# Performance work log

Measured on AMD Instinct MI355X. Metric: run time of the kernel, lower is better.

Reference implementation:

```python
import jax, jax.numpy as jnp
import numpy as np

B, D_IN, RANK, UNITS = 8192, 4096, 2048, 4096

def setup_inputs() -> dict:
    key = jax.random.key(0)
    k1, k2, k3, k4 = jax.random.split(key, 4)
    inputs = jax.random.normal(k1, (B, D_IN), dtype=jnp.float32)
    U = jax.random.normal(k2, (D_IN, RANK), dtype=jnp.float32) / np.sqrt(D_IN)
    S = jax.random.uniform(k3, (RANK,), dtype=jnp.float32)
    V = jax.random.normal(k4, (UNITS, RANK), dtype=jnp.float32) / np.sqrt(UNITS)
    bias = jnp.zeros((UNITS,), dtype=jnp.float32)
    return {"inputs": inputs, "U": U, "S": S, "V": V, "bias": bias}

def reference(inputs, U, S, V, bias):
    # kernel = U @ diag(S) @ V^T; out = relu(inputs @ kernel + bias)
    # Computed in factored form (same math, avoids dense [D_IN, UNITS] kernel):
    h = (inputs @ U) * S            # [B, rank]
    out = h @ V.T + bias            # [B, units]
    return jax.nn.relu(out)
```

## Files before the change

### kernel.cpp

```cpp
#include <hip/hip_runtime.h>
#include <hip/hip_bf16.h>

#define BSZ   8192
#define DIN   4096
#define RNK   2048
#define UNT   4096

typedef __attribute__((ext_vector_type(4))) float  f32x4;
typedef __attribute__((ext_vector_type(8))) float  f32x8;
typedef __attribute__((ext_vector_type(8))) short  s16x8;
typedef __attribute__((ext_vector_type(8))) unsigned short u16x8;

typedef unsigned short u16;

__device__ __forceinline__ u16 f2bf(float f) {
    unsigned int u = __builtin_bit_cast(unsigned int, f);
    return (u16)((u + 0x7fffu + ((u >> 16) & 1u)) >> 16);
}

__global__ void cvt_bf16_kernel(const float* __restrict__ x,
                                u16* __restrict__ y, int n8) {
    int i = blockIdx.x * blockDim.x + threadIdx.x;
    if (i >= n8) return;
    f32x8 v = ((const f32x8*)x)[i];
    u16x8 o;
#pragma unroll
    for (int j = 0; j < 8; ++j) o[j] = f2bf(v[j]);
    ((u16x8*)y)[i] = o;
}

__global__ void transpose_scale_kernel(const float* __restrict__ U,
                                       const float* __restrict__ S,
                                       u16* __restrict__ Ut) {
    __shared__ float tile[32][33];
    const int r0 = blockIdx.x * 32;
    const int k0 = blockIdx.y * 32;
    const int tx = threadIdx.x;
    const int ty = threadIdx.y;
#pragma unroll
    for (int i = 0; i < 32; i += 8)
        tile[ty + i][tx] = U[(size_t)(k0 + ty + i) * RNK + r0 + tx];
    __syncthreads();
#pragma unroll
    for (int i = 0; i < 32; i += 8) {
        int r = r0 + ty + i;
        Ut[(size_t)r * DIN + k0 + tx] = f2bf(tile[tx][ty + i] * S[r]);
    }
}

__device__ __forceinline__ void glds16(const void* g, void* l) {
    __builtin_amdgcn_global_load_lds(
        (const __attribute__((address_space(1))) unsigned int*)g,
        (__attribute__((address_space(3))) unsigned int*)l,
        16, 0, 0);
}

template <int K, bool RELU_BIAS>
__global__ __launch_bounds__(256) void gemm_bt(
    const u16* __restrict__ A, const u16* __restrict__ Bt,
    void* __restrict__ C, const float* __restrict__ bias, int N) {
    __shared__ u16 As[2][128 * 32];
    __shared__ u16 Bs[2][128 * 32];

    const int t    = threadIdx.x;
    const int wave = t >> 6;
    const int lane = t & 63;

    const int rowBase = blockIdx.y * 128;
    const int colBase = blockIdx.x * 128;

    const int sRow = t >> 2;
    const int sCol = (t & 3) * 8;
    const u16* aG = A  + (size_t)(rowBase + sRow) * K + sCol;
    const u16* bG = Bt + (size_t)(colBase + sRow) * K + sCol;
    const int lo = sRow * 32 + sCol;
    const int hi = (sRow + 64) * 32 + sCol;

    const int wm = (wave >> 1) * 64;
    const int wn = (wave & 1) * 64;
    const int fr = lane & 15;
    const int fk = (lane >> 4) * 8;

    const int fOff = (wm + fr) * 32 + fk;
    const int gOff = (wn + fr) * 32 + fk;

    f32x4 acc[4][4] = {};

    for (int k0 = 0; k0 < K; k0 += 64) {
        __syncthreads();
        glds16(aG + k0,                       &As[0][lo]);
        glds16(aG + (size_t)64 * K + k0,      &As[0][hi]);
        glds16(aG + k0 + 32,                  &As[1][lo]);
        glds16(aG + (size_t)64 * K + k0 + 32, &As[1][hi]);
        glds16(bG + k0,                       &Bs[0][lo]);
        glds16(bG + (size_t)64 * K + k0,      &Bs[0][hi]);
        glds16(bG + k0 + 32,                  &Bs[1][lo]);
        glds16(bG + (size_t)64 * K + k0 + 32, &Bs[1][hi]);
        __syncthreads();

#pragma unroll
        for (int h = 0; h < 2; ++h) {
            const u16* aF = &As[h][fOff];
            const u16* bF = &Bs[h][gOff];
            s16x8 af[4], bf[4];
#pragma unroll
            for (int i = 0; i < 4; ++i) af[i] = *(const s16x8*)(aF + i * 16 * 32);
#pragma unroll
            for (int j = 0; j < 4; ++j) bf[j] = *(const s16x8*)(bF + j * 16 * 32);
#pragma unroll
            for (int i = 0; i < 4; ++i)
#pragma unroll
                for (int j = 0; j < 4; ++j)
                    acc[i][j] = __builtin_amdgcn_mfma_f32_16x16x32_bf16(
                        af[i], bf[j], acc[i][j], 0, 0, 0);
        }
    }

    const int cRow = rowBase + wm + (lane >> 4) * 4;
    const int cCol = colBase + wn + fr;
    if (RELU_BIAS) {
        float* Cf = (float*)C;
#pragma unroll
        for (int j = 0; j < 4; ++j) {
            const int col = cCol + j * 16;
            const float bv = bias[col];
#pragma unroll
            for (int i = 0; i < 4; ++i) {
#pragma unroll
                for (int r = 0; r < 4; ++r) {
                    float v = acc[i][j][r] + bv;
                    Cf[(size_t)(cRow + i * 16 + r) * N + col] = v > 0.f ? v : 0.f;
                }
            }
        }
    } else {
        u16* Cb = (u16*)C;
#pragma unroll
        for (int j = 0; j < 4; ++j) {
            const int col = cCol + j * 16;
#pragma unroll
            for (int i = 0; i < 4; ++i) {
#pragma unroll
                for (int r = 0; r < 4; ++r)
                    Cb[(size_t)(cRow + i * 16 + r) * N + col] = f2bf(acc[i][j][r]);
            }
        }
    }
}

extern "C" void kernel_launch(void* const* d_in, const int* in_sizes, int n_in,
                              void* d_out, int out_size, void* d_ws, size_t ws_size,
                              hipStream_t stream) {
    const float* X    = (const float*)d_in[0];
    const float* U    = (const float*)d_in[1];
    const float* S    = (const float*)d_in[2];
    const float* V    = (const float*)d_in[3];
    const float* bias = (const float*)d_in[4];
    float* out = (float*)d_out;

    char* ws = (char*)d_ws;
    u16* Xb  = (u16*)ws;
    u16* Utb = (u16*)(ws + ((size_t)64 << 20));
    u16* Vb  = (u16*)(ws + ((size_t)80 << 20));
    u16* Hb  = (u16*)(ws + ((size_t)96 << 20));

    {
        int n8 = (BSZ * DIN) / 8;
        cvt_bf16_kernel<<<n8 / 256, 256, 0, stream>>>(X, Xb, n8);
    }
    {
        dim3 grid(RNK / 32, DIN / 32), block(32, 8);
        transpose_scale_kernel<<<grid, block, 0, stream>>>(U, S, Utb);
    }
    {
        int n8 = (UNT * RNK) / 8;
        cvt_bf16_kernel<<<n8 / 256, 256, 0, stream>>>(V, Vb, n8);
    }
    {
        dim3 grid(RNK / 128, BSZ / 128);
        gemm_bt<DIN, false><<<grid, 256, 0, stream>>>(Xb, Utb, Hb, nullptr, RNK);
    }
    {
        dim3 grid(UNT / 128, BSZ / 128);
        gemm_bt<RNK, true><<<grid, 256, 0, stream>>>(Hb, Vb, out, bias, UNT);
    }
}
```

Baseline: 569.3 us.

## Replace 128x128 GEMM with 256x256 tile, 8-wave pipelined swizzled kernel

Rewrites the bf16 GEMM kernel to use 256x256 output tiles with 512 threads and a K step of 64. The LDS layout is XOR-swizzled to avoid bank conflicts, and global-to-LDS prefetch is staggered across four MFMA phases with barriers and raised wave priority. Workgroup IDs are remapped for better L2 locality. The aim is to raise arithmetic intensity and overlap loads with MFMA, at the cost of 128KB of LDS and higher register pressure, which may limit occupancy.

```diff
diff --git a/kernel.cpp b/kernel.cpp
--- a/kernel.cpp
+++ b/kernel.cpp
@@ -56,93 +56,183 @@
 }
 
 template <int K, bool RELU_BIAS>
-__global__ __launch_bounds__(256) void gemm_bt(
+__global__ __launch_bounds__(512) void gemm256(
     const u16* __restrict__ A, const u16* __restrict__ Bt,
     void* __restrict__ C, const float* __restrict__ bias, int N) {
-    __shared__ u16 As[2][128 * 32];
-    __shared__ u16 Bs[2][128 * 32];
-
-    const int t    = threadIdx.x;
+    __shared__ u16 As[2][256 * 64];
+    __shared__ u16 Bs[2][256 * 64];
+
+    const int t = threadIdx.x;
+
+    const int gx = gridDim.x;
+    const int nwg = gx * gridDim.y;
+    int bid = blockIdx.y * gx + blockIdx.x;
+    bid = (bid & 7) * (nwg >> 3) + (bid >> 3);
+    const int rowBase = (bid / gx) * 256;
+    const int colBase = (bid % gx) * 256;
+
+    const int sRow = t >> 3;
+    const int sCol = ((t & 7) ^ (sRow & 7)) << 3;
+    const u16* aS = A  + (size_t)(rowBase + sRow) * K + sCol;
+    const u16* bS = Bt + (size_t)(colBase + sRow) * K + sCol;
+
+#define STG(SRC, DST, h_, Tk_, b_) do {                                       \
+    const u16* s_ = (SRC) + (size_t)(h_) * 128 * K + (size_t)(Tk_) * 64;      \
+    glds16(s_,                  &DST[b_][(h_) * 8192 + t * 8]);               \
+    glds16(s_ + (size_t)64 * K, &DST[b_][(h_) * 8192 + 4096 + t * 8]);        \
+} while (0)
+
+    const int lane = t & 63;
     const int wave = t >> 6;
-    const int lane = t & 63;
-
-    const int rowBase = blockIdx.y * 128;
-    const int colBase = blockIdx.x * 128;
-
-    const int sRow = t >> 2;
-    const int sCol = (t & 3) * 8;
-    const u16* aG = A  + (size_t)(rowBase + sRow) * K + sCol;
-    const u16* bG = Bt + (size_t)(colBase + sRow) * K + sCol;
-    const int lo = sRow * 32 + sCol;
-    const int hi = (sRow + 64) * 32 + sCol;
-
-    const int wm = (wave >> 1) * 64;
-    const int wn = (wave & 1) * 64;
-    const int fr = lane & 15;
-    const int fk = (lane >> 4) * 8;
-
-    const int fOff = (wm + fr) * 32 + fk;
-    const int gOff = (wn + fr) * 32 + fk;
-
-    f32x4 acc[4][4] = {};
-
-    for (int k0 = 0; k0 < K; k0 += 64) {
-        __syncthreads();
-        glds16(aG + k0,                       &As[0][lo]);
-        glds16(aG + (size_t)64 * K + k0,      &As[0][hi]);
-        glds16(aG + k0 + 32,                  &As[1][lo]);
-        glds16(aG + (size_t)64 * K + k0 + 32, &As[1][hi]);
-        glds16(bG + k0,                       &Bs[0][lo]);
-        glds16(bG + (size_t)64 * K + k0,      &Bs[0][hi]);
-        glds16(bG + k0 + 32,                  &Bs[1][lo]);
-        glds16(bG + (size_t)64 * K + k0 + 32, &Bs[1][hi]);
-        __syncthreads();
-
-#pragma unroll
-        for (int h = 0; h < 2; ++h) {
-            const u16* aF = &As[h][fOff];
-            const u16* bF = &Bs[h][gOff];
-            s16x8 af[4], bf[4];
-#pragma unroll
-            for (int i = 0; i < 4; ++i) af[i] = *(const s16x8*)(aF + i * 16 * 32);
-#pragma unroll
-            for (int j = 0; j < 4; ++j) bf[j] = *(const s16x8*)(bF + j * 16 * 32);
-#pragma unroll
-            for (int i = 0; i < 4; ++i)
-#pragma unroll
-                for (int j = 0; j < 4; ++j)
-                    acc[i][j] = __builtin_amdgcn_mfma_f32_16x16x32_bf16(
-                        af[i], bf[j], acc[i][j], 0, 0, 0);
-        }
-    }
-
-    const int cRow = rowBase + wm + (lane >> 4) * 4;
-    const int cCol = colBase + wn + fr;
+    const int wm = wave >> 2;
+    const int wn = wave & 3;
+    const int lr = lane & 15;
+    const int lg = lane >> 4;
+    const int r7 = lr & 7;
+    const int swz0 = ((lg    ) ^ r7) << 4;
+    const int swz1 = ((lg + 4) ^ r7) << 4;
+    const int aRowB = (wm * 128 + lr) * 128;
+    const int bRowB = (wn * 64  + lr) * 128;
+
+    f32x4 acc[8][4] = {};
+    s16x8 af[8][2], bf[2][2];
+
+    STG(aS, As, 0, 0, 0); STG(aS, As, 1, 0, 0);
+    STG(bS, Bs, 0, 0, 0); STG(bS, Bs, 1, 0, 0);
+    STG(aS, As, 0, 1, 1); STG(aS, As, 1, 1, 1);
+    asm volatile("s_waitcnt vmcnt(4)" ::: "memory");
+    __builtin_amdgcn_s_barrier();
+
+    const int NT = K / 64;
+    for (int T = 0; T < NT; ++T) {
+        const int cur = T & 1, nxt = cur ^ 1;
+        const char* aP = (const char*)&As[cur][0] + aRowB;
+        const char* bP = (const char*)&Bs[cur][0] + bRowB;
+
+#pragma unroll
+        for (int mi = 0; mi < 4; ++mi) {
+            af[mi][0] = *(const s16x8*)(aP + mi * 2048 + swz0);
+            af[mi][1] = *(const s16x8*)(aP + mi * 2048 + swz1);
+        }
+#pragma unroll
+        for (int nj = 0; nj < 2; ++nj) {
+            bf[nj][0] = *(const s16x8*)(bP + nj * 2048 + swz0);
+            bf[nj][1] = *(const s16x8*)(bP + nj * 2048 + swz1);
+        }
+        if (T + 1 < NT) STG(bS, Bs, 0, T + 1, nxt);
+        asm volatile("" ::: "memory");
+        __builtin_amdgcn_s_barrier();
+        asm volatile("s_waitcnt lgkmcnt(0)" ::: "memory");
+        __builtin_amdgcn_sched_barrier(0);
+        __builtin_amdgcn_s_setprio(1);
+#pragma unroll
+        for (int mi = 0; mi < 4; ++mi)
+#pragma unroll
+            for (int nj = 0; nj < 2; ++nj)
+#pragma unroll
+                for (int kk = 0; kk < 2; ++kk)
+                    acc[mi][nj] = __builtin_amdgcn_mfma_f32_16x16x32_bf16(
+                        af[mi][kk], bf[nj][kk], acc[mi][nj], 0, 0, 0);
+        __builtin_amdgcn_s_setprio(0);
+        asm volatile("" ::: "memory");
+        __builtin_amdgcn_s_barrier();
+
+#pragma unroll
+        for (int mi = 0; mi < 4; ++mi) {
+            af[4 + mi][0] = *(const s16x8*)(aP + (4 + mi) * 2048 + swz0);
+            af[4 + mi][1] = *(const s16x8*)(aP + (4 + mi) * 2048 + swz1);
+        }
+        if (T + 1 < NT) STG(bS, Bs, 1, T + 1, nxt);
+        asm volatile("" ::: "memory");
+        __builtin_amdgcn_s_barrier();
+        asm volatile("s_waitcnt lgkmcnt(0)" ::: "memory");
+        __builtin_amdgcn_sched_barrier(0);
+        __builtin_amdgcn_s_setprio(1);
+#pragma unroll
+        for (int mi = 0; mi < 4; ++mi)
+#pragma unroll
+            for (int nj = 0; nj < 2; ++nj)
+#pragma unroll
+                for (int kk = 0; kk < 2; ++kk)
+                    acc[4 + mi][nj] = __builtin_amdgcn_mfma_f32_16x16x32_bf16(
+                        af[4 + mi][kk], bf[nj][kk], acc[4 + mi][nj], 0, 0, 0);
+        __builtin_amdgcn_s_setprio(0);
+        asm volatile("" ::: "memory");
+        __builtin_amdgcn_s_barrier();
+
+#pragma unroll
+        for (int nj = 0; nj < 2; ++nj) {
+            bf[nj][0] = *(const s16x8*)(bP + (2 + nj) * 2048 + swz0);
+            bf[nj][1] = *(const s16x8*)(bP + (2 + nj) * 2048 + swz1);
+        }
+        if (T + 2 < NT) STG(aS, As, 0, T + 2, cur);
+        asm volatile("" ::: "memory");
+        __builtin_amdgcn_s_barrier();
+        asm volatile("s_waitcnt lgkmcnt(0)" ::: "memory");
+        __builtin_amdgcn_sched_barrier(0);
+        __builtin_amdgcn_s_setprio(1);
+#pragma unroll
+        for (int mi = 0; mi < 4; ++mi)
+#pragma unroll
+            for (int nj = 0; nj < 2; ++nj)
+#pragma unroll
+                for (int kk = 0; kk < 2; ++kk)
+                    acc[mi][2 + nj] = __builtin_amdgcn_mfma_f32_16x16x32_bf16(
+                        af[mi][kk], bf[nj][kk], acc[mi][2 + nj], 0, 0, 0);
+        __builtin_amdgcn_s_setprio(0);
+        asm volatile("" ::: "memory");
+        __builtin_amdgcn_s_barrier();
+
+        if (T + 2 < NT) STG(aS, As, 1, T + 2, cur);
+        asm volatile("" ::: "memory");
+        __builtin_amdgcn_s_barrier();
+        __builtin_amdgcn_s_setprio(1);
+#pragma unroll
+        for (int mi = 0; mi < 4; ++mi)
+#pragma unroll
+            for (int nj = 0; nj < 2; ++nj)
+#pragma unroll
+                for (int kk = 0; kk < 2; ++kk)
+                    acc[4 + mi][2 + nj] = __builtin_amdgcn_mfma_f32_16x16x32_bf16(
+                        af[4 + mi][kk], bf[nj][kk], acc[4 + mi][2 + nj], 0, 0, 0);
+        __builtin_amdgcn_s_setprio(0);
+        if (T + 2 < NT) {
+            asm volatile("s_waitcnt vmcnt(4)" ::: "memory");
+        } else if (T + 1 < NT) {
+            asm volatile("s_waitcnt vmcnt(0)" ::: "memory");
+        }
+        asm volatile("" ::: "memory");
+        __builtin_amdgcn_s_barrier();
+    }
+#undef STG
+
+    const int cRow = rowBase + wm * 128 + lg * 4;
+    const int cCol = colBase + wn * 64 + lr;
     if (RELU_BIAS) {
         float* Cf = (float*)C;
 #pragma unroll
-        for (int j = 0; j < 4; ++j) {
-            const int col = cCol + j * 16;
+        for (int n = 0; n < 4; ++n) {
+            const int col = cCol + n * 16;
             const float bv = bias[col];
 #pragma unroll
-            for (int i = 0; i < 4; ++i) {
+            for (int m = 0; m < 8; ++m) {
 #pragma unroll
                 for (int r = 0; r < 4; ++r) {
-                    float v = acc[i][j][r] + bv;
-                    Cf[(size_t)(cRow + i * 16 + r) * N + col] = v > 0.f ? v : 0.f;
+                    float v = acc[m][n][r] + bv;
+                    Cf[(size_t)(cRow + m * 16 + r) * N + col] = v > 0.f ? v : 0.f;
                 }
             }
         }
     } else {
         u16* Cb = (u16*)C;
 #pragma unroll
-        for (int j = 0; j < 4; ++j) {
-            const int col = cCol + j * 16;
-#pragma unroll
-            for (int i = 0; i < 4; ++i) {
+        for (int n = 0; n < 4; ++n) {
+            const int col = cCol + n * 16;
+#pragma unroll
+            for (int m = 0; m < 8; ++m) {
 #pragma unroll
                 for (int r = 0; r < 4; ++r)
-                    Cb[(size_t)(cRow + i * 16 + r) * N + col] = f2bf(acc[i][j][r]);
+                    Cb[(size_t)(cRow + m * 16 + r) * N + col] = f2bf(acc[m][n][r]);
             }
         }
     }
@@ -177,11 +267,11 @@
         cvt_bf16_kernel<<<n8 / 256, 256, 0, stream>>>(V, Vb, n8);
     }
     {
-        dim3 grid(RNK / 128, BSZ / 128);
-        gemm_bt<DIN, false><<<grid, 256, 0, stream>>>(Xb, Utb, Hb, nullptr, RNK);
-    }
-    {
-        dim3 grid(UNT / 128, BSZ / 128);
-        gemm_bt<RNK, true><<<grid, 256, 0, stream>>>(Hb, Vb, out, bias, UNT);
-    }
-}
+        dim3 grid(RNK / 256, BSZ / 256);
+        gemm256<DIN, false><<<grid, 512, 0, stream>>>(Xb, Utb, Hb, nullptr, RNK);
+    }
+    {
+        dim3 grid(UNT / 256, BSZ / 256);
+        gemm256<RNK, true><<<grid, 512, 0, stream>>>(Hb, Vb, out, bias, UNT);
+    }
+}
```

New measurement: 576.9 us. Within noise of the previous version (+1.3%).
